# Performance work log

Hardware: AMD Instinct MI355X
Metric: run time of the kernel (lower is better)

Reference implementation:

```python
import jax, jax.numpy as jnp
import numpy as np

N = 25000              # nodes
E = 400000             # edges (avg degree 16)
MUL_S, MUL_V = 64, 32  # irreps_hidden = 64x0e + 32x1o
NB, NH = 8, 64         # num_basis, invariant_neurons
WNUM = 64 + 64 + 32 + 32 + 32  # tp.weight_numel over the 5 uvu paths = 224
AVG_NEI = 16.0
EPS = 1e-5
INV_SQRT3 = 1.0 / np.sqrt(3.0)
INV_SQRT2 = 1.0 / np.sqrt(2.0)


def setup_inputs():
    key = jax.random.key(0)
    ks = jax.random.split(key, 16)
    inp = {}
    inp['node_hiddens'] = jax.random.normal(ks[0], (N, MUL_S + 3 * MUL_V), jnp.float32)
    inp['edge_index'] = jax.random.randint(ks[1], (2, E), 0, N)
    inp['edge_sh'] = jax.random.normal(ks[2], (E, 4), jnp.float32)
    inp['edge_attr'] = jax.random.uniform(ks[3], (E, NB), jnp.float32)
    # linear_1 (per-irrep block mixing)
    inp['W1_0'] = jax.random.normal(ks[4], (MUL_S, MUL_S), jnp.float32)
    inp['W1_1'] = jax.random.normal(ks[5], (MUL_V, MUL_V), jnp.float32)
    # radial MLP [8,64,64,224]
    inp['Wfc1'] = jax.random.normal(ks[6], (NB, NH), jnp.float32)
    inp['Wfc2'] = jax.random.normal(ks[7], (NH, NH), jnp.float32)
    inp['Wfc3'] = jax.random.normal(ks[8], (NH, WNUM), jnp.float32)
    # linear_2: irreps_mid.simplify() = 96x0e + 128x1o -> 64x0e + 32x1o
    inp['W2_0'] = jax.random.normal(ks[9], (96, MUL_S), jnp.float32)
    inp['W2_1'] = jax.random.normal(ks[10], (128, MUL_V), jnp.float32)
    # self-connection linear
    inp['Wsc0'] = jax.random.normal(ks[11], (MUL_S, MUL_S), jnp.float32)
    inp['Wsc1'] = jax.random.normal(ks[12], (MUL_V, MUL_V), jnp.float32)
    # equivariant layernorm affine weights (centering=False -> no bias)
    inp['g0'] = jnp.ones((MUL_S,), jnp.float32)
    inp['g1'] = jnp.ones((MUL_V,), jnp.float32)
    return inp


def _split(x):
    return x[:, :MUL_S], x[:, MUL_S:].reshape(-1, MUL_V, 3)


def _forward(node_hiddens, edge_sh, edge_attr, W1_0, W1_1, Wfc1, Wfc2, Wfc3,
             W2_0, W2_1, Wsc0, Wsc1, g0, g1, edge_src, edge_dst):
    s_in, v_in = _split(node_hiddens)
    # self-connection (e3nn Linear: weight / sqrt(fan_in))
    sc_s = (s_in @ Wsc0) / np.sqrt(MUL_S)
    sc_v = jnp.einsum('nuc,uv->nvc', v_in, Wsc1) / np.sqrt(MUL_V)
    # linear_1
    s = (s_in @ W1_0) / np.sqrt(MUL_S)
    v = jnp.einsum('nuc,uv->nvc', v_in, W1_1) / np.sqrt(MUL_V)
    # radial MLP -> per-edge tensor-product weights [E, 224]
    h = jax.nn.silu(edge_attr @ Wfc1 / np.sqrt(NB))
    h = jax.nn.silu(h @ Wfc2 / np.sqrt(NH))
    w = h @ Wfc3 / np.sqrt(NH)
    w0, w1, w2 = w[:, :64], w[:, 64:128], w[:, 128:160]
    w3, w4 = w[:, 160:192], w[:, 192:224]
    # gather destination node features per edge
    sd = s[edge_dst]            # [E, 64]
    vd = v[edge_dst]            # [E, 32, 3]
    sh0 = edge_sh[:, :1]        # l=0 component
    sh1 = edge_sh[:, 1:4]       # l=1 components
    # uvu tensor-product paths (CG coeffs folded with e3nn component path weights)
    m0 = w0 * sd * sh0                                          # 0e x 0e -> 0e
    m1 = w3 * jnp.sum(vd * sh1[:, None, :], -1) * INV_SQRT3     # 1o x 1o -> 0e
    mv0 = (w1 * sd)[:, :, None] * sh1[:, None, :]               # 0e x 1o -> 1o
    mv1 = w2[:, :, None] * vd * sh0[:, :, None]                 # 1o x 0e -> 1o
    sh1b = jnp.broadcast_to(sh1[:, None, :], vd.shape)
    mv2 = w4[:, :, None] * jnp.cross(vd, sh1b) * INV_SQRT2      # 1o x 1o -> 1o
    mid_s = jnp.concatenate([m0, m1], -1)          # [E, 96]
    mid_v = jnp.concatenate([mv0, mv1, mv2], 1)    # [E, 128, 3]
    # scatter-sum to source nodes, divide by sqrt(avg_num_neighbors)
    ns = jax.ops.segment_sum(mid_s, edge_src, num_segments=N) / np.sqrt(AVG_NEI)
    nv = jax.ops.segment_sum(mid_v, edge_src, num_segments=N) / np.sqrt(AVG_NEI)
    # linear_2 + residual self-connection
    out_s = (ns @ W2_0) / np.sqrt(96) + sc_s
    out_v = jnp.einsum('nuc,uv->nvc', nv, W2_1) / np.sqrt(128) + sc_v
    # equivariant RMS layernorm (centering=False), per irrep block
    rms_s = jnp.sqrt(jnp.mean(out_s ** 2, -1, keepdims=True) + EPS)
    out_s = out_s / rms_s * g0
    rms_v = jnp.sqrt(jnp.mean(jnp.sum(out_v ** 2, -1), -1) + EPS)  # mean over mul of |v|^2
    out_v = out_v / rms_v[:, None, None] * g1[None, :, None]
    return jnp.concatenate([out_s, out_v.reshape(-1, 3 * MUL_V)], -1)


def reference(node_hiddens, edge_index, edge_sh, edge_attr, W1_0, W1_1,
              Wfc1, Wfc2, Wfc3, W2_0, W2_1, Wsc0, Wsc1, g0, g1):
    edge_src = edge_index[0]
    edge_dst = edge_index[1]
    return _forward(node_hiddens, edge_sh, edge_attr, W1_0, W1_1, Wfc1, Wfc2,
                    Wfc3, W2_0, W2_1, Wsc0, Wsc1, g0, g1, edge_src, edge_dst)
```

## Files before the change

kernel.cpp:

```cpp
#include <hip/hip_runtime.h>
#include <hip/hip_fp16.h>

#define N_NODES 25000
#define N_EDGES 400000
#define EPS_F 1e-5f

typedef _Float16 f16x8 __attribute__((ext_vector_type(8)));
typedef _Float16 f16x4 __attribute__((ext_vector_type(4)));
typedef float    f32x4 __attribute__((ext_vector_type(4)));
typedef unsigned int uint;

__device__ __forceinline__ float silu_f(float x) {
    return x / (1.0f + __expf(-x));
}

__global__ __launch_bounds__(256) void k_prepack(
    const float* __restrict__ Wfc1, const float* __restrict__ Wfc2,
    const float* __restrict__ Wfc3,
    _Float16* __restrict__ gA1, _Float16* __restrict__ gA2,
    _Float16* __restrict__ gA3)
{
    int t = blockIdx.x * 256 + threadIdx.x;
    int L = t & 63, q = L >> 4, cc = L & 15;
    if (t < 256) {
        int nt = t >> 6;
        f16x8 p;
#pragma unroll
        for (int j = 0; j < 8; ++j)
            p[j] = (q == 0) ? (_Float16)Wfc1[j*64 + nt*16 + cc] : (_Float16)0.f;
        *(f16x8*)&gA1[t*8] = p;
    } else if (t < 768) {
        int tt = t - 256;
        int tile = tt >> 6, ks = tile >> 2, nt = tile & 3;
        int kb = ks*32 + q*8;
        f16x8 p;
#pragma unroll
        for (int j = 0; j < 8; ++j)
            p[j] = (_Float16)Wfc2[(kb+j)*64 + nt*16 + cc];
        *(f16x8*)&gA2[tt*8] = p;
    } else if (t < 2560) {
        int tt = t - 768;
        int tile = tt >> 6, ks = tile / 14, nt = tile - ks*14;
        int kb = ks*32 + q*8;
        f16x8 p;
#pragma unroll
        for (int j = 0; j < 8; ++j)
            p[j] = (_Float16)Wfc3[(kb+j)*224 + nt*16 + cc];
        *(f16x8*)&gA3[tt*8] = p;
    }
}

__global__ __launch_bounds__(256) void k_node_pre(
    const float* __restrict__ nh,
    const float* __restrict__ W1_0, const float* __restrict__ W1_1,
    const float* __restrict__ Wsc0, const float* __restrict__ Wsc1,
    float* __restrict__ XS, float* __restrict__ SC)
{
    int lane = threadIdx.x & 63, wv = threadIdx.x >> 6;
    int n = blockIdx.x*4 + wv;
    if (n >= N_NODES) return;
    int u_ = lane & 31;
    bool lo = lane < 32;
    const float* row = nh + n*160;

    float sval = row[lane];
    float vx = row[64 + u_*3 + 0];
    float vy = row[64 + u_*3 + 1];
    float vz = row[64 + u_*3 + 2];

    float as = 0.f, bs = 0.f;
#pragma unroll 4
    for (int k = 0; k < 64; ++k) {
        float sk = __shfl(sval, k);
        as += sk * W1_0[k*64 + lane];
        bs += sk * Wsc0[k*64 + lane];
    }
    float* xsrow = XS + n*192;
    float* scrow = SC + n*192;
    xsrow[lane] = as * 0.125f;
    scrow[lane] = bs * 0.125f;

    float selv = lo ? vx : vz;
    int srcbase = lane & 32;
    float aP=0.f, aQ=0.f, bP=0.f, bQ=0.f;
#pragma unroll 4
    for (int u = 0; u < 32; ++u) {
        float su = __shfl(selv, u | srcbase);
        float sy = __shfl(vy, u);
        float wa = W1_1[u*32 + u_];
        float wb = Wsc1[u*32 + u_];
        aP += su*wa; aQ += sy*wa;
        bP += su*wb; bQ += sy*wb;
    }
    const float is32 = 0.17677669529663687f;
    if (lo) {
        xsrow[64 + u_*4 + 0] = aP * is32;
        xsrow[64 + u_*4 + 1] = aQ * is32;
        scrow[64 + u_*4 + 0] = bP * is32;
        scrow[64 + u_*4 + 1] = bQ * is32;
    } else {
        xsrow[64 + u_*4 + 2] = aP * is32;
        scrow[64 + u_*4 + 2] = bP * is32;
    }
}

__global__ __launch_bounds__(256) void k_build_lists(
    const int* __restrict__ ei, int* __restrict__ CNT, int* __restrict__ LIST)
{
    int e = blockIdx.x * 256 + threadIdx.x;
    if (e >= N_EDGES) return;
    int src = ei[e];
    int pos = atomicAdd(&CNT[src], 1);
    if (pos < 64) LIST[src*64 + pos] = e;
}

__global__ __launch_bounds__(256, 4) void k_edge_mlp(
    const float* __restrict__ eat,
    const _Float16* __restrict__ gA1, const _Float16* __restrict__ gA2,
    const _Float16* __restrict__ gA3,
    uint* __restrict__ WP)
{
    __shared__ _Float16 h1b[64*72];
    __shared__ _Float16 h2b[64*72];

    const int tid = threadIdx.x;
    const int lane = tid & 63, wv = tid >> 6;
    const int q = lane >> 4, col = lane & 15;
    const int erow = wv*16 + col;
    const int ecol = blockIdx.x*64 + erow;

    const float IS8 = 0.35355339059327373f;

    f16x8 b1;
#pragma unroll
    for (int j = 0; j < 8; ++j) b1[j] = (_Float16)0.f;
    if (q == 0) {
        float4 v0 = *(const float4*)(eat + (size_t)ecol*8);
        float4 v1 = *(const float4*)(eat + (size_t)ecol*8 + 4);
        b1[0]=(_Float16)v0.x; b1[1]=(_Float16)v0.y; b1[2]=(_Float16)v0.z; b1[3]=(_Float16)v0.w;
        b1[4]=(_Float16)v1.x; b1[5]=(_Float16)v1.y; b1[6]=(_Float16)v1.z; b1[7]=(_Float16)v1.w;
    }
#pragma unroll
    for (int nt = 0; nt < 4; ++nt) {
        f32x4 acc = {0.f,0.f,0.f,0.f};
        f16x8 a = *(const f16x8*)&gA1[(nt*64 + lane)*8];
        acc = __builtin_amdgcn_mfma_f32_16x16x32_f16(a, b1, acc, 0, 0, 0);
        f16x4 p;
#pragma unroll
        for (int r = 0; r < 4; ++r) p[r] = (_Float16)silu_f(acc[r]*IS8);
        *(f16x4*)&h1b[erow*72 + nt*16 + q*4] = p;
    }
#pragma unroll
    for (int nt = 0; nt < 4; ++nt) {
        f32x4 acc = {0.f,0.f,0.f,0.f};
#pragma unroll
        for (int ks = 0; ks < 2; ++ks) {
            f16x8 a = *(const f16x8*)&gA2[((ks*4+nt)*64 + lane)*8];
            f16x8 b = *(const f16x8*)&h1b[erow*72 + ks*32 + q*8];
            acc = __builtin_amdgcn_mfma_f32_16x16x32_f16(a, b, acc, 0, 0, 0);
        }
        f16x4 p;
#pragma unroll
        for (int r = 0; r < 4; ++r) p[r] = (_Float16)silu_f(acc[r]*0.125f);
        *(f16x4*)&h2b[erow*72 + nt*16 + q*4] = p;
    }
    uint* wpE = WP + (size_t)ecol*128;
    auto tileAcc = [&](int nt) -> f32x4 {
        f32x4 acc = {0.f,0.f,0.f,0.f};
#pragma unroll
        for (int ks = 0; ks < 2; ++ks) {
            f16x8 a = *(const f16x8*)&gA3[((ks*14+nt)*64 + lane)*8];
            f16x8 b = *(const f16x8*)&h2b[erow*72 + ks*32 + q*8];
            acc = __builtin_amdgcn_mfma_f32_16x16x32_f16(a, b, acc, 0, 0, 0);
        }
        return acc;
    };
    auto packStore = [&](f32x4 A, f32x4 B, int baseIdx) {
        uint d[4];
#pragma unroll
        for (int r = 0; r < 4; ++r) {
            __half2 h = __floats2half2_rn(A[r]*0.125f, B[r]*0.125f);
            d[r] = *(uint*)&h;
        }
        *(uint4*)&wpE[baseIdx + q*4] = make_uint4(d[0], d[1], d[2], d[3]);
    };
    f32x4 t10 = tileAcc(10);
    f32x4 t11 = tileAcc(11);
    packStore(tileAcc(0),  tileAcc(4),  0);
    packStore(tileAcc(1),  tileAcc(5),  16);
    packStore(tileAcc(2),  tileAcc(6),  32);
    packStore(tileAcc(3),  tileAcc(7),  48);
    packStore(tileAcc(8),  t10,         64);
    packStore(tileAcc(9),  t11,         80);
    packStore(tileAcc(12), t10,         96);
    packStore(tileAcc(13), t11,        112);
}

struct Pref { float4 sh, vv; float sd; uint wa, wb; };

__device__ __forceinline__ void preload(
    Pref& P, int e, int dst,
    const float* __restrict__ esh, const uint* __restrict__ WP,
    const float* __restrict__ XS, int lane, int u_)
{
    P.sh = *(const float4*)(esh + (size_t)e*4);
    const uint* wp = WP + (size_t)e*128;
    P.wa = wp[lane];
    P.wb = wp[64 + lane];
    const float* xd = XS + (size_t)dst*192;
    P.sd = xd[lane];
    P.vv = *(const float4*)(xd + 64 + u_*4);
}

__global__ __launch_bounds__(256) void k_aggregate(
    const int* __restrict__ ei, const float* __restrict__ esh,
    const uint* __restrict__ WP, const float* __restrict__ XS,
    const float* __restrict__ SC, const int* __restrict__ CNT,
    const int* __restrict__ LIST,
    const float* __restrict__ W2_0, const float* __restrict__ W2_1,
    const float* __restrict__ g0, const float* __restrict__ g1,
    float* __restrict__ out)
{
    __shared__ float aSb[2][2][96];
    __shared__ float aVb[2][2][392];
    int tid = threadIdx.x;
    int lane = tid & 63, wv = tid >> 6;
    int n2 = wv >> 1, half = wv & 1;
    int n = blockIdx.x*2 + n2;
    int u_ = lane & 31;
    bool lo = lane < 32;

    int cnt; { int c = CNT[n]; cnt = c > 64 ? 64 : c; }
    const int* edst = ei + N_EDGES;

    int e_l = 0, dst_l = 0;
    if (cnt > 0) {
        int li = lane < cnt ? lane : cnt - 1;
        e_l = LIST[n*64 + li];
        dst_l = edst[e_l];
    }

    float accM0=0, aV0x=0, aV0y=0, aV0z=0, accM1=0, a12x=0, a12y=0, a12z=0;

    Pref P;
    int i = half;
    if (i < cnt) preload(P, __shfl(e_l,i), __shfl(dst_l,i), esh, WP, XS, lane, u_);
#pragma unroll 1
    for (; i < cnt; i += 2) {
        Pref cur = P;
        int nx = i + 2;
        if (nx < cnt) preload(P, __shfl(e_l,nx), __shfl(dst_l,nx), esh, WP, XS, lane, u_);
        float2 f01 = __half22float2(*(const __half2*)&cur.wa);
        float2 fAB = __half22float2(*(const __half2*)&cur.wb);
        accM0 += f01.x*cur.sd*cur.sh.x;
        float t1 = f01.y*cur.sd;
        aV0x += t1*cur.sh.y; aV0y += t1*cur.sh.z; aV0z += t1*cur.sh.w;
        if (lo) {
            accM1 += fAB.y*(cur.vv.x*cur.sh.y + cur.vv.y*cur.sh.z + cur.vv.z*cur.sh.w);
            a12x += fAB.x*cur.vv.x*cur.sh.x;
            a12y += fAB.x*cur.vv.y*cur.sh.x;
            a12z += fAB.x*cur.vv.z*cur.sh.x;
        } else {
            a12x += fAB.x*(cur.vv.y*cur.sh.w - cur.vv.z*cur.sh.z);
            a12y += fAB.x*(cur.vv.z*cur.sh.y - cur.vv.x*cur.sh.w);
            a12z += fAB.x*(cur.vv.x*cur.sh.z - cur.vv.y*cur.sh.y);
        }
    }

    const float SEG = 0.25f;
    const float IS3 = 0.5773502691896258f;
    const float IS2 = 0.7071067811865476f;
    aSb[n2][half][lane] = accM0 * SEG;
    aVb[n2][half][0*130 + lane] = aV0x * SEG;
    aVb[n2][half][1*130 + lane] = aV0y * SEG;
    aVb[n2][half][2*130 + lane] = aV0z * SEG;
    if (lo) {
        aSb[n2][half][64 + u_] = accM1 * SEG * IS3;
        aVb[n2][half][0*130 + 64 + u_] = a12x * SEG;
        aVb[n2][half][1*130 + 64 + u_] = a12y * SEG;
        aVb[n2][half][2*130 + 64 + u_] = a12z * SEG;
    } else {
        aVb[n2][half][0*130 + 96 + u_] = a12x * SEG * IS2;
        aVb[n2][half][1*130 + 96 + u_] = a12y * SEG * IS2;
        aVb[n2][half][2*130 + 96 + u_] = a12z * SEG * IS2;
    }
    __syncthreads();

    if (half == 0) {
        aSb[n2][0][lane] += aSb[n2][1][lane];
        if (lo) aSb[n2][0][64 + u_] += aSb[n2][1][64 + u_];

        float o0=0,o1=0,o2=0,o3=0;
#pragma unroll 4
        for (int k = 0; k < 96; k += 4) {
            o0 += aSb[n2][0][k+0] * W2_0[(k+0)*64 + lane];
            o1 += aSb[n2][0][k+1] * W2_0[(k+1)*64 + lane];
            o2 += aSb[n2][0][k+2] * W2_0[(k+2)*64 + lane];
            o3 += aSb[n2][0][k+3] * W2_0[(k+3)*64 + lane];
        }
        float os = (o0+o1)+(o2+o3);
        const float IS96 = 0.10206207261596575f;
        os = os*IS96 + SC[n*192 + lane];

        float r = os*os;
#pragma unroll
        for (int off = 32; off > 0; off >>= 1) r += __shfl_xor(r, off);
        float rms_s = sqrtf(r*(1.0f/64.0f) + EPS_F);
        out[(size_t)n*160 + lane] = os / rms_s * g0[lane];
    } else {
        for (int idx = lane; idx < 392; idx += 64)
            aVb[n2][0][idx] += aVb[n2][1][idx];

        int coff = lo ? 0 : 2*130;
        float p0=0,p1=0,q0=0,q1=0;
#pragma unroll 4
        for (int u = 0; u < 128; u += 2) {
            float wv0 = W2_1[(u+0)*32 + u_];
            float wv1 = W2_1[(u+1)*32 + u_];
            p0 += aVb[n2][0][coff + u+0]*wv0;  q0 += aVb[n2][0][130 + u+0]*wv0;
            p1 += aVb[n2][0][coff + u+1]*wv1;  q1 += aVb[n2][0][130 + u+1]*wv1;
        }
        float ov0 = p0+p1, ov1 = q0+q1;
        const float IS128 = 0.08838834764831845f;
        float4 scv = *(const float4*)(SC + n*192 + 64 + u_*4);
        float x0 = ov0*IS128 + (lo ? scv.x : scv.z);
        float x1 = ov1*IS128 + scv.y;

        float rv = lo ? (x0*x0 + x1*x1) : (x0*x0);
#pragma unroll
        for (int off = 32; off > 0; off >>= 1) rv += __shfl_xor(rv, off);
        float rms_v = sqrtf(rv*(1.0f/32.0f) + EPS_F);

        float* orow = out + (size_t)n*160;
        float gv = g1[u_] / rms_v;
        if (lo) {
            orow[64 + u_*3 + 0] = x0 * gv;
            orow[64 + u_*3 + 1] = x1 * gv;
        } else {
            orow[64 + u_*3 + 2] = x0 * gv;
        }
    }
}

extern "C" void kernel_launch(void* const* d_in, const int* in_sizes, int n_in,
                              void* d_out, int out_size, void* d_ws, size_t ws_size,
                              hipStream_t stream)
{
    const float* nh   = (const float*)d_in[0];
    const int*   ei   = (const int*)  d_in[1];
    const float* esh  = (const float*)d_in[2];
    const float* eat  = (const float*)d_in[3];
    const float* W1_0 = (const float*)d_in[4];
    const float* W1_1 = (const float*)d_in[5];
    const float* Wfc1 = (const float*)d_in[6];
    const float* Wfc2 = (const float*)d_in[7];
    const float* Wfc3 = (const float*)d_in[8];
    const float* W2_0 = (const float*)d_in[9];
    const float* W2_1 = (const float*)d_in[10];
    const float* Wsc0 = (const float*)d_in[11];
    const float* Wsc1 = (const float*)d_in[12];
    const float* g0   = (const float*)d_in[13];
    const float* g1   = (const float*)d_in[14];
    float* out = (float*)d_out;

    char* base = (char*)d_ws;
    float*    XS   = (float*)base;
    float*    SC   = XS + (size_t)N_NODES*192;
    uint*     WP   = (uint*)(SC + (size_t)N_NODES*192);
    _Float16* gA1  = (_Float16*)(WP + (size_t)N_EDGES*128);
    _Float16* gA2  = gA1 + 2048;
    _Float16* gA3  = gA2 + 4096;
    int*      CNT  = (int*)(gA3 + 14336);
    int*      LIST = CNT + N_NODES;

    hipMemsetAsync(CNT, 0, N_NODES*sizeof(int), stream);
    k_prepack   <<<10, 256, 0, stream>>>(Wfc1, Wfc2, Wfc3, gA1, gA2, gA3);
    k_node_pre  <<<(N_NODES+3)/4, 256, 0, stream>>>(nh, W1_0, W1_1, Wsc0, Wsc1, XS, SC);
    k_build_lists<<<(N_EDGES+255)/256, 256, 0, stream>>>(ei, CNT, LIST);
    k_edge_mlp  <<<N_EDGES/64, 256, 0, stream>>>(eat, gA1, gA2, gA3, WP);
    k_aggregate <<<N_NODES/2, 256, 0, stream>>>(ei, esh, WP, XS, SC, CNT, LIST,
                                                W2_0, W2_1, g0, g1, out);
}
```

Baseline: 369.0 us.

## Build CSR edge ordering and write edge data in source-sorted slots

Replaces the per-node fixed-64 edge lists with a CSR layout built by a count kernel, a single-block prefix scan and a fill kernel. The edge MLP writes its per-edge weights straight into source-sorted slots, and spherical harmonics and destination indices are permuted the same way, so aggregation reads contiguous memory instead of gathering by edge id. It adds two extra launches, including a serial single-block scan, plus scattered writes in the MLP and fill kernels. The cap of 64 edges per node is still applied when aggregating.

```diff
diff --git a/kernel.cpp b/kernel.cpp
--- a/kernel.cpp
+++ b/kernel.cpp
@@ -104,18 +104,60 @@
     }
 }
 
-__global__ __launch_bounds__(256) void k_build_lists(
-    const int* __restrict__ ei, int* __restrict__ CNT, int* __restrict__ LIST)
+__global__ __launch_bounds__(256) void k_count(
+    const int* __restrict__ ei, int* __restrict__ CNT)
+{
+    int e = blockIdx.x * 256 + threadIdx.x;
+    if (e >= N_EDGES) return;
+    atomicAdd(&CNT[ei[e]], 1);
+}
+
+__global__ __launch_bounds__(256) void k_scan(
+    const int* __restrict__ CNT, int* __restrict__ ROWP)
+{
+    __shared__ int wsum[4];
+    const int CH = (N_NODES + 255) / 256;
+    int tid = threadIdx.x;
+    int lane = tid & 63, wv = tid >> 6;
+    int base = tid * CH;
+    int s = 0;
+    for (int j = 0; j < CH; ++j) {
+        int idx = base + j;
+        if (idx < N_NODES) s += CNT[idx];
+    }
+    int inc = s;
+    for (int off = 1; off < 64; off <<= 1) {
+        int o = __shfl_up(inc, off);
+        if (lane >= off) inc += o;
+    }
+    if (lane == 63) wsum[wv] = inc;
+    __syncthreads();
+    int woff = 0;
+    for (int w = 0; w < wv; ++w) woff += wsum[w];
+    int run = woff + inc - s;
+    for (int j = 0; j < CH; ++j) {
+        int idx = base + j;
+        if (idx < N_NODES) { ROWP[idx] = run; run += CNT[idx]; }
+    }
+}
+
+__global__ __launch_bounds__(256) void k_fill(
+    const int* __restrict__ ei, const float* __restrict__ esh,
+    const int* __restrict__ ROWP, int* __restrict__ CNT2,
+    int* __restrict__ SLOT, int* __restrict__ DSTP, float* __restrict__ SHP)
 {
     int e = blockIdx.x * 256 + threadIdx.x;
     if (e >= N_EDGES) return;
     int src = ei[e];
-    int pos = atomicAdd(&CNT[src], 1);
-    if (pos < 64) LIST[src*64 + pos] = e;
+    int pos = atomicAdd(&CNT2[src], 1);
+    int slot = ROWP[src] + pos;
+    SLOT[e] = slot;
+    DSTP[slot] = ei[N_EDGES + e];
+    *(float4*)(SHP + (size_t)slot*4) = *(const float4*)(esh + (size_t)e*4);
 }
 
 __global__ __launch_bounds__(256, 4) void k_edge_mlp(
-    const float* __restrict__ eat,
+    const float* __restrict__ eat, const int* __restrict__ SLOT,
     const _Float16* __restrict__ gA1, const _Float16* __restrict__ gA2,
     const _Float16* __restrict__ gA3,
     uint* __restrict__ WP)
@@ -164,7 +206,8 @@
         for (int r = 0; r < 4; ++r) p[r] = (_Float16)silu_f(acc[r]*0.125f);
         *(f16x4*)&h2b[erow*72 + nt*16 + q*4] = p;
     }
-    uint* wpE = WP + (size_t)ecol*128;
+    int slot = SLOT[ecol];
+    uint* wpE = WP + (size_t)slot*128;
     auto tileAcc = [&](int nt) -> f32x4 {
         f32x4 acc = {0.f,0.f,0.f,0.f};
 #pragma unroll
@@ -199,12 +242,12 @@
 struct Pref { float4 sh, vv; float sd; uint wa, wb; };
 
 __device__ __forceinline__ void preload(
-    Pref& P, int e, int dst,
-    const float* __restrict__ esh, const uint* __restrict__ WP,
+    Pref& P, int slot, int dst,
+    const float* __restrict__ SHP, const uint* __restrict__ WP,
     const float* __restrict__ XS, int lane, int u_)
 {
-    P.sh = *(const float4*)(esh + (size_t)e*4);
-    const uint* wp = WP + (size_t)e*128;
+    P.sh = *(const float4*)(SHP + (size_t)slot*4);
+    const uint* wp = WP + (size_t)slot*128;
     P.wa = wp[lane];
     P.wb = wp[64 + lane];
     const float* xd = XS + (size_t)dst*192;
@@ -213,10 +256,10 @@
 }
 
 __global__ __launch_bounds__(256) void k_aggregate(
-    const int* __restrict__ ei, const float* __restrict__ esh,
-    const uint* __restrict__ WP, const float* __restrict__ XS,
+    const uint* __restrict__ WP, const float* __restrict__ SHP,
+    const int* __restrict__ DSTP, const float* __restrict__ XS,
     const float* __restrict__ SC, const int* __restrict__ CNT,
-    const int* __restrict__ LIST,
+    const int* __restrict__ ROWP,
     const float* __restrict__ W2_0, const float* __restrict__ W2_1,
     const float* __restrict__ g0, const float* __restrict__ g1,
     float* __restrict__ out)
@@ -231,25 +274,21 @@
     bool lo = lane < 32;
 
     int cnt; { int c = CNT[n]; cnt = c > 64 ? 64 : c; }
-    const int* edst = ei + N_EDGES;
-
-    int e_l = 0, dst_l = 0;
-    if (cnt > 0) {
-        int li = lane < cnt ? lane : cnt - 1;
-        e_l = LIST[n*64 + li];
-        dst_l = edst[e_l];
-    }
+    int base = ROWP[n];
+
+    int dst_l = 0;
+    if (lane < cnt) dst_l = DSTP[base + lane];
 
     float accM0=0, aV0x=0, aV0y=0, aV0z=0, accM1=0, a12x=0, a12y=0, a12z=0;
 
     Pref P;
     int i = half;
-    if (i < cnt) preload(P, __shfl(e_l,i), __shfl(dst_l,i), esh, WP, XS, lane, u_);
+    if (i < cnt) preload(P, base+i, __shfl(dst_l,i), SHP, WP, XS, lane, u_);
 #pragma unroll 1
     for (; i < cnt; i += 2) {
         Pref cur = P;
         int nx = i + 2;
-        if (nx < cnt) preload(P, __shfl(e_l,nx), __shfl(dst_l,nx), esh, WP, XS, lane, u_);
+        if (nx < cnt) preload(P, base+nx, __shfl(dst_l,nx), SHP, WP, XS, lane, u_);
         float2 f01 = __half22float2(*(const __half2*)&cur.wa);
         float2 fAB = __half22float2(*(const __half2*)&cur.wb);
         accM0 += f01.x*cur.sd*cur.sh.x;
@@ -367,17 +406,24 @@
     float*    XS   = (float*)base;
     float*    SC   = XS + (size_t)N_NODES*192;
     uint*     WP   = (uint*)(SC + (size_t)N_NODES*192);
-    _Float16* gA1  = (_Float16*)(WP + (size_t)N_EDGES*128);
+    float*    SHP  = (float*)(WP + (size_t)N_EDGES*128);
+    _Float16* gA1  = (_Float16*)(SHP + (size_t)N_EDGES*4);
     _Float16* gA2  = gA1 + 2048;
     _Float16* gA3  = gA2 + 4096;
     int*      CNT  = (int*)(gA3 + 14336);
-    int*      LIST = CNT + N_NODES;
-
-    hipMemsetAsync(CNT, 0, N_NODES*sizeof(int), stream);
-    k_prepack   <<<10, 256, 0, stream>>>(Wfc1, Wfc2, Wfc3, gA1, gA2, gA3);
-    k_node_pre  <<<(N_NODES+3)/4, 256, 0, stream>>>(nh, W1_0, W1_1, Wsc0, Wsc1, XS, SC);
-    k_build_lists<<<(N_EDGES+255)/256, 256, 0, stream>>>(ei, CNT, LIST);
-    k_edge_mlp  <<<N_EDGES/64, 256, 0, stream>>>(eat, gA1, gA2, gA3, WP);
-    k_aggregate <<<N_NODES/2, 256, 0, stream>>>(ei, esh, WP, XS, SC, CNT, LIST,
-                                                W2_0, W2_1, g0, g1, out);
-}
+    int*      CNT2 = CNT + N_NODES;
+    int*      ROWP = CNT2 + N_NODES;
+    int*      SLOT = ROWP + N_NODES;
+    int*      DSTP = SLOT + N_EDGES;
+
+    hipMemsetAsync(CNT, 0, 2*N_NODES*sizeof(int), stream);
+    k_prepack <<<10, 256, 0, stream>>>(Wfc1, Wfc2, Wfc3, gA1, gA2, gA3);
+    k_count   <<<(N_EDGES+255)/256, 256, 0, stream>>>(ei, CNT);
+    k_scan    <<<1, 256, 0, stream>>>(CNT, ROWP);
+    k_fill    <<<(N_EDGES+255)/256, 256, 0, stream>>>(ei, esh, ROWP, CNT2,
+                                                      SLOT, DSTP, SHP);
+    k_node_pre<<<(N_NODES+3)/4, 256, 0, stream>>>(nh, W1_0, W1_1, Wsc0, Wsc1, XS, SC);
+    k_edge_mlp<<<N_EDGES/64, 256, 0, stream>>>(eat, SLOT, gA1, gA2, gA3, WP);
+    k_aggregate<<<N_NODES/2, 256, 0, stream>>>(WP, SHP, DSTP, XS, SC, CNT, ROWP,
+                                               W2_0, W2_1, g0, g1, out);
+}
```

New measurement: 444.5 us. 20.4% more time.
